# Kernel optimization log

Measured on AMD Instinct MI355X. Metric: run time of the kernel, lower is better.

## Reference

```python
import jax, jax.numpy as jnp
import numpy as np

NUM_USERS = 100000
NUM_ITEMS = 50000
NUM_LAYERS = 4
DIM_H = 64
E_HALF = 2000000  # undirected interactions; symmetrized to 4M directed edges


def setup_inputs() -> dict:
    key = jax.random.key(0)
    k1, k2, k3, k4 = jax.random.split(key, 4)
    emb_users = 0.01 * jax.random.normal(k1, (NUM_USERS, DIM_H), dtype=jnp.float32)
    emb_items = 0.01 * jax.random.normal(k2, (NUM_ITEMS, DIM_H), dtype=jnp.float32)
    u = jax.random.randint(k3, (E_HALF,), 0, NUM_USERS, dtype=jnp.int64)
    it = jax.random.randint(k4, (E_HALF,), 0, NUM_ITEMS, dtype=jnp.int64) + NUM_USERS
    # bidirectional bipartite graph, as LightGCN expects
    src = jnp.concatenate([u, it])
    dst = jnp.concatenate([it, u])
    edge_index = jnp.stack([src, dst])  # [2, 4M]
    return {"emb_users": emb_users, "emb_items": emb_items, "edge_index": edge_index}


def reference(emb_users, emb_items, edge_index):
    N = emb_users.shape[0] + emb_items.shape[0]
    src, dst = edge_index[0], edge_index[1]
    # gcn_norm (add_self_loops=False): w_e = deg[src]^-1/2 * deg[dst]^-1/2
    deg = jax.ops.segment_sum(jnp.ones(src.shape[0], dtype=emb_users.dtype), dst, num_segments=N)
    dis = jnp.where(deg > 0, deg ** -0.5, 0.0).astype(emb_users.dtype)
    w = (dis[src] * dis[dst])[:, None]  # [E,1]

    emb = jnp.concatenate([emb_users, emb_items])  # [N, D]
    embs_sum = emb
    x = emb
    for _ in range(NUM_LAYERS):
        x = jax.ops.segment_sum(w * x[src], dst, num_segments=N)  # LGConv
        embs_sum = embs_sum + x
    # original: 1/(L+1) * mean over L+1 stacked layers -> sum / (L+1)^2
    emb_final = embs_sum / float((NUM_LAYERS + 1) ** 2)
    emb_users_final = emb_final[: emb_users.shape[0]]
    emb_items_final = emb_final[emb_users.shape[0]:]
    return (emb_users_final, emb_users, emb_items_final, emb_items)
```

## Files before the change

### kernel.cpp

```cpp
#include <hip/hip_runtime.h>
#include <hip/hip_fp8.h>

typedef unsigned char u8;
typedef float v2f __attribute__((ext_vector_type(2)));

#define SCAN_B 256

#define NPB      128
#define NPB_SH   7
#define P2_CAP   6144
#define STG_CAP  6144
#define P1_CHUNK 8192
#define NB_MAX   2048
#define STG_OFF  ((size_t)10 << 20)

static __device__ __forceinline__ float fp8_to_f32(u8 b) {
    __hip_fp8_e4m3 t;
    t.__x = (__hip_fp8_storage_t)b;
    return (float)t;
}
static __device__ __forceinline__ u8 f32_to_fp8(float v) {
    __hip_fp8_e4m3 t(v);
    return (u8)t.__x;
}

template <bool HI>
static __device__ __forceinline__ v2f pk2(unsigned w) {
#if __has_builtin(__builtin_amdgcn_cvt_pk_f32_fp8)
    return __builtin_amdgcn_cvt_pk_f32_fp8((int)w, HI);
#else
    v2f r;
    r.x = fp8_to_f32(HI ? (u8)(w >> 16) : (u8)(w));
    r.y = fp8_to_f32(HI ? (u8)(w >> 24) : (u8)(w >> 8));
    return r;
#endif
}

__global__ void detect_kernel(const int* __restrict__ edges, int* __restrict__ flag) {
    __shared__ int cnt[256];
    int t = threadIdx.x;
    int c = 0;
    for (int i = t; i < 32768; i += 256)
        if (edges[2 * i + 1] != 0) c++;
    cnt[t] = c;
    __syncthreads();
    for (int off = 128; off > 0; off >>= 1) {
        if (t < off) cnt[t] += cnt[t + off];
        __syncthreads();
    }
    if (t == 0) flag[0] = (cnt[0] < 8) ? 2 : 1;
}

__global__ void gcur_fixed_init(int* __restrict__ gcur, int NB) {
    int b = blockIdx.x * blockDim.x + threadIdx.x;
    if (b < NB) gcur[b] = b * STG_CAP;
}

__global__ void part1_kernel(const int* __restrict__ edges, const int* __restrict__ flag,
                             int* __restrict__ gcur, int2* __restrict__ staging,
                             int E, int NB) {
    __shared__ int lcount[NB_MAX];
    __shared__ int lbase[NB_MAX];
    int t = threadIdx.x;
    int s = flag[0];
    long e0 = (long)blockIdx.x * P1_CHUNK;
    for (int b = t; b < NB; b += 256) lcount[b] = 0;
    __syncthreads();
    for (int j = 0; j < P1_CHUNK / 256; ++j) {
        long e = e0 + j * 256 + t;
        if (e < E) {
            int dv = edges[(long)E * s + e * s];
            atomicAdd(&lcount[dv >> NPB_SH], 1);
        }
    }
    __syncthreads();
    for (int b = t; b < NB; b += 256) {
        int c = lcount[b];
        lbase[b] = (c > 0) ? atomicAdd(&gcur[b], c) : 0;
        lcount[b] = 0;
    }
    __syncthreads();
    for (int j = 0; j < P1_CHUNK / 256; ++j) {
        long e = e0 + j * 256 + t;
        if (e < E) {
            int sv = edges[e * s];
            int dv = edges[(long)E * s + e * s];
            int b = dv >> NPB_SH;
            int slot = atomicAdd(&lcount[b], 1);
            int pos = lbase[b] + slot;
            if (pos < (b + 1) * STG_CAP)
                staging[pos] = make_int2(sv, dv);
        }
    }
}

__global__ void bucket_scan_kernel(const int* __restrict__ gcur, int* __restrict__ bbase,
                                   int NB) {
    __shared__ int sh[2][1024];
    int t = threadIdx.x;
    int i0 = 2 * t, i1 = 2 * t + 1;
    int a0 = (i0 < NB) ? (gcur[i0] - i0 * STG_CAP) : 0;
    int a1 = (i1 < NB) ? (gcur[i1] - i1 * STG_CAP) : 0;
    sh[0][t] = a0 + a1;
    __syncthreads();
    int src = 0;
    for (int off = 1; off < 1024; off <<= 1) {
        int x = sh[src][t] + ((t >= off) ? sh[src][t - off] : 0);
        sh[src ^ 1][t] = x;
        src ^= 1;
        __syncthreads();
    }
    int incl = sh[src][t];
    int excl = incl - (a0 + a1);
    if (i0 < NB) bbase[i0] = excl;
    if (i1 < NB) bbase[i1] = excl + a0;
    if (t == 1023) bbase[NB] = incl;
}

__global__ void __launch_bounds__(256) part2a_kernel(
        const int* __restrict__ gcur, const int* __restrict__ bbase,
        const int2* __restrict__ staging, int* __restrict__ row_ptr,
        float* __restrict__ dis, int n, int E, int NB) {
    __shared__ int cnt[NPB];
    __shared__ int sc[2][NPB];
    int b = blockIdx.x;
    int t = threadIdx.x;
    int dlo = b << NPB_SH;
    int sbase = b * STG_CAP;
    int c = gcur[b] - sbase;
    int base = bbase[b];
    if (t < NPB) cnt[t] = 0;
    __syncthreads();
    for (int k = t; k < c; k += 256) {
        int2 sd = staging[sbase + k];
        atomicAdd(&cnt[sd.y - dlo], 1);
    }
    __syncthreads();
    if (t < NPB) sc[0][t] = cnt[t];
    __syncthreads();
    int src = 0;
    for (int off = 1; off < NPB; off <<= 1) {
        if (t < NPB) {
            int x = sc[src][t] + ((t >= off) ? sc[src][t - off] : 0);
            sc[src ^ 1][t] = x;
        }
        src ^= 1;
        __syncthreads();
    }
    if (t < NPB) {
        int node = dlo + t;
        if (node < n) {
            int d = cnt[t];
            row_ptr[node] = base + sc[src][t] - d;
            dis[node] = (d > 0) ? rsqrtf((float)d) : 0.0f;
        }
    }
    if (b == 0 && t == 0) row_ptr[n] = E;
}

__global__ void __launch_bounds__(256) part2b_kernel(
        const int* __restrict__ row_ptr, const int* __restrict__ gcur,
        const int2* __restrict__ staging, const float* __restrict__ dis,
        int2* __restrict__ cw, int n) {
    __shared__ int2 win[P2_CAP];
    __shared__ int cur[NPB];
    int b = blockIdx.x;
    int t = threadIdx.x;
    int dlo = b << NPB_SH;
    int sbase = b * STG_CAP;
    int cnt = gcur[b] - sbase;
    int base = row_ptr[dlo];
    if (t < NPB) {
        int node = dlo + t;
        cur[t] = (node < n) ? (row_ptr[node] - base) : 0;
    }
    __syncthreads();
    if (cnt <= P2_CAP) {
        for (int k = t; k < cnt; k += 256) {
            int2 sd = staging[sbase + k];
            float w = dis[sd.x] * dis[sd.y];
            int p = atomicAdd(&cur[sd.y - dlo], 1);
            win[p] = make_int2(sd.x, __float_as_int(w));
        }
        __syncthreads();
        for (int k = t; k < cnt; k += 256)
            cw[base + k] = win[k];
    } else {
        for (int k = t; k < cnt; k += 256) {
            int2 sd = staging[sbase + k];
            float w = dis[sd.x] * dis[sd.y];
            int p = atomicAdd(&cur[sd.y - dlo], 1);
            cw[base + p] = make_int2(sd.x, __float_as_int(w));
        }
    }
}

__global__ void count_deg_kernel(const int* __restrict__ edges, const int* __restrict__ flag,
                                 int* __restrict__ deg, int E) {
    int e = blockIdx.x * blockDim.x + threadIdx.x;
    if (e >= E) return;
    int s = flag[0];
    int d = edges[(long)E * s + (long)e * s];
    atomicAdd(&deg[d], 1);
}

__global__ void scan_phase1(const int* __restrict__ deg, int* __restrict__ row_ptr,
                            int* __restrict__ bsum, int n) {
    __shared__ int sh[2][SCAN_B];
    int t = threadIdx.x;
    int gi = blockIdx.x * SCAN_B + t;
    int v = (gi < n) ? deg[gi] : 0;
    int src = 0;
    sh[0][t] = v;
    __syncthreads();
    for (int off = 1; off < SCAN_B; off <<= 1) {
        int x = sh[src][t] + ((t >= off) ? sh[src][t - off] : 0);
        sh[src ^ 1][t] = x;
        src ^= 1;
        __syncthreads();
    }
    int incl = sh[src][t];
    if (gi < n) row_ptr[gi] = incl - v;
    if (t == SCAN_B - 1) bsum[blockIdx.x] = incl;
}

__global__ void scan_phase2(int* __restrict__ bsum, int nb) {
    __shared__ int sh[1024];
    int t = threadIdx.x;
    sh[t] = (t < nb) ? bsum[t] : 0;
    __syncthreads();
    if (t == 0) {
        int acc = 0;
        for (int i = 0; i < nb; ++i) { int x = sh[i]; sh[i] = acc; acc += x; }
    }
    __syncthreads();
    if (t < nb) bsum[t] = sh[t];
}

__global__ void scan_phase3(const int* __restrict__ deg, const int* __restrict__ bsum,
                            int* __restrict__ row_ptr, int* __restrict__ cursor,
                            float* __restrict__ dis, int n, int E) {
    int gi = blockIdx.x * SCAN_B + threadIdx.x;
    if (gi < n) {
        int e = row_ptr[gi] + bsum[blockIdx.x];
        row_ptr[gi] = e;
        cursor[gi]  = e;
        int d = deg[gi];
        dis[gi] = (d > 0) ? rsqrtf((float)d) : 0.0f;
    }
    if (gi == 0) row_ptr[n] = E;
}

__global__ void scatter_kernel(const int* __restrict__ edges, const int* __restrict__ flag,
                               const float* __restrict__ dis, int* __restrict__ cursor,
                               int2* __restrict__ cw, int E) {
    int e = blockIdx.x * blockDim.x + threadIdx.x;
    if (e >= E) return;
    int s = flag[0];
    int sv = edges[(long)e * s];
    int dv = edges[(long)E * s + (long)e * s];
    float w = dis[sv] * dis[dv];
    int pos = atomicAdd(&cursor[dv], 1);
    cw[pos] = make_int2(sv, __float_as_int(w));
}

__global__ void init_kernel(const float* __restrict__ eu, const float* __restrict__ ei,
                            u8* __restrict__ x0, long NU64, long tot) {
    long i = (long)blockIdx.x * blockDim.x + threadIdx.x;
    if (i >= tot) return;
    float v = (i < NU64) ? eu[i] : ei[i - NU64];
    x0[i] = f32_to_fp8(v);
}

__global__ void spmm_kernel(const int* __restrict__ row_ptr, const int2* __restrict__ cw,
                            const u8* __restrict__ xin, u8* __restrict__ xout, int n) {
    int wave = (blockIdx.x * blockDim.x + threadIdx.x) >> 6;
    int lane = threadIdx.x & 63;
    if (wave >= n) return;
    int beg = row_ptr[wave], end = row_ptr[wave + 1];
    int g = lane >> 3;
    int h = lane & 7;

    float a0 = 0.f, a1 = 0.f, a2 = 0.f, a3 = 0.f;
    float a4 = 0.f, a5 = 0.f, a6 = 0.f, a7 = 0.f;

    for (int iA = beg + g; iA < end; iA += 16) {
        int iB = iA + 8;
        bool vB = iB < end;

        int2 ca = cw[iA];
        int2 cb = cw[vB ? iB : iA];

        uint2 dA = *(const uint2*)(xin + ((long)ca.x << 6) + (h << 3));
        uint2 dB = *(const uint2*)(xin + ((long)cb.x << 6) + (h << 3));

        float wA = __int_as_float(ca.y);
        float wB = vB ? __int_as_float(cb.y) : 0.0f;

        v2f pA0 = pk2<false>(dA.x), pA1 = pk2<true>(dA.x);
        v2f pA2 = pk2<false>(dA.y), pA3 = pk2<true>(dA.y);
        v2f pB0 = pk2<false>(dB.x), pB1 = pk2<true>(dB.x);
        v2f pB2 = pk2<false>(dB.y), pB3 = pk2<true>(dB.y);

        a0 = fmaf(wA, pA0.x, a0); a1 = fmaf(wA, pA0.y, a1);
        a2 = fmaf(wA, pA1.x, a2); a3 = fmaf(wA, pA1.y, a3);
        a4 = fmaf(wA, pA2.x, a4); a5 = fmaf(wA, pA2.y, a5);
        a6 = fmaf(wA, pA3.x, a6); a7 = fmaf(wA, pA3.y, a7);
        a0 = fmaf(wB, pB0.x, a0); a1 = fmaf(wB, pB0.y, a1);
        a2 = fmaf(wB, pB1.x, a2); a3 = fmaf(wB, pB1.y, a3);
        a4 = fmaf(wB, pB2.x, a4); a5 = fmaf(wB, pB2.y, a5);
        a6 = fmaf(wB, pB3.x, a6); a7 = fmaf(wB, pB3.y, a7);
    }

    a0 += __shfl_xor(a0, 8);  a1 += __shfl_xor(a1, 8);
    a2 += __shfl_xor(a2, 8);  a3 += __shfl_xor(a3, 8);
    a4 += __shfl_xor(a4, 8);  a5 += __shfl_xor(a5, 8);
    a6 += __shfl_xor(a6, 8);  a7 += __shfl_xor(a7, 8);
    a0 += __shfl_xor(a0, 16); a1 += __shfl_xor(a1, 16);
    a2 += __shfl_xor(a2, 16); a3 += __shfl_xor(a3, 16);
    a4 += __shfl_xor(a4, 16); a5 += __shfl_xor(a5, 16);
    a6 += __shfl_xor(a6, 16); a7 += __shfl_xor(a7, 16);
    a0 += __shfl_xor(a0, 32); a1 += __shfl_xor(a1, 32);
    a2 += __shfl_xor(a2, 32); a3 += __shfl_xor(a3, 32);
    a4 += __shfl_xor(a4, 32); a5 += __shfl_xor(a5, 32);
    a6 += __shfl_xor(a6, 32); a7 += __shfl_xor(a7, 32);

    if (g == 0) {
        unsigned lo = (unsigned)f32_to_fp8(a0)
                    | ((unsigned)f32_to_fp8(a1) << 8)
                    | ((unsigned)f32_to_fp8(a2) << 16)
                    | ((unsigned)f32_to_fp8(a3) << 24);
        unsigned hi = (unsigned)f32_to_fp8(a4)
                    | ((unsigned)f32_to_fp8(a5) << 8)
                    | ((unsigned)f32_to_fp8(a6) << 16)
                    | ((unsigned)f32_to_fp8(a7) << 24);
        *(uint2*)(xout + ((long)wave << 6) + (h << 3)) = make_uint2(lo, hi);
    }
}

__global__ void final_kernel(const u8* __restrict__ x1, const u8* __restrict__ x2,
                             const u8* __restrict__ x3, const u8* __restrict__ x4,
                             const float* __restrict__ eu, const float* __restrict__ ei,
                             float* __restrict__ out, long NU64, long NI64) {
    long i = (long)blockIdx.x * blockDim.x + threadIdx.x;
    if (i >= NU64 + NI64) return;
    float base = (i < NU64) ? eu[i] : ei[i - NU64];
    float s = base + fp8_to_f32(x1[i]) + fp8_to_f32(x2[i])
                   + fp8_to_f32(x3[i]) + fp8_to_f32(x4[i]);
    float v = s * (1.0f / 25.0f);
    if (i < NU64) {
        out[i] = v;
        out[NU64 + i] = base;
    } else {
        long j = i - NU64;
        out[2 * NU64 + j] = v;
        out[2 * NU64 + NI64 + j] = base;
    }
}

extern "C" void kernel_launch(void* const* d_in, const int* in_sizes, int n_in,
                              void* d_out, int out_size, void* d_ws, size_t ws_size,
                              hipStream_t stream) {
    const float* eu = (const float*)d_in[0];
    const float* ei = (const float*)d_in[1];
    const int* edges = (const int*)d_in[2];
    float* out = (float*)d_out;

    const int NU = in_sizes[0] / 64;
    const int NI = in_sizes[1] / 64;
    const int N  = NU + NI;
    const int E  = in_sizes[2] / 2;
    const int NB = (N + NPB - 1) / NPB;

    char* w = (char*)d_ws;
    size_t off = 0;
    auto alloc = [&](size_t bytes) -> void* {
        void* p = w + off;
        off += (bytes + 255) & ~(size_t)255;
        return p;
    };
    int*   flag    = (int*)  alloc(256);
    int*   deg     = (int*)  alloc((size_t)N * 4);
    int*   row_ptr = (int*)  alloc((size_t)(N + 1) * 4);
    int*   cursor  = (int*)  alloc((size_t)N * 4);
    float* dis     = (float*)alloc((size_t)N * 4);
    int*   bsum    = (int*)  alloc(1024 * 4);
    int*   gcur    = (int*)  alloc((size_t)(NB + 1) * 4);
    int*   bbase   = (int*)  alloc((size_t)(NB + 1) * 4);
    int2*  cw      = (int2*) alloc((size_t)E * 8);
    const long NU64 = (long)NU * 64, NI64 = (long)NI * 64;
    const long tot = NU64 + NI64;
    u8* x1 = (u8*)alloc((size_t)tot);
    u8* x2 = (u8*)alloc((size_t)tot);
    u8* x3 = (u8*)alloc((size_t)tot);
    u8* x4 = (u8*)alloc((size_t)tot);

    const size_t out_bytes = (size_t)tot * 8;
    u8*   x0      = (u8*)out;
    int2* staging = (int2*)((char*)out + STG_OFF);

    detect_kernel<<<1, 256, 0, stream>>>(edges, flag);

    bool fast = (NB <= NB_MAX) &&
                (STG_OFF + (size_t)NB * STG_CAP * 8 <= out_bytes) &&
                ((size_t)tot <= STG_OFF);

    if (fast) {
        gcur_fixed_init<<<(NB + 255) / 256, 256, 0, stream>>>(gcur, NB);
        part1_kernel<<<(E + P1_CHUNK - 1) / P1_CHUNK, 256, 0, stream>>>(edges, flag, gcur,
                                                                        staging, E, NB);
        bucket_scan_kernel<<<1, 1024, 0, stream>>>(gcur, bbase, NB);
        part2a_kernel<<<NB, 256, 0, stream>>>(gcur, bbase, staging, row_ptr, dis, N, E, NB);
        part2b_kernel<<<NB, 256, 0, stream>>>(row_ptr, gcur, staging, dis, cw, N);
    } else {
        const int nb = (N + SCAN_B - 1) / SCAN_B;
        hipMemsetAsync(deg, 0, (size_t)N * 4, stream);
        count_deg_kernel<<<(E + 255) / 256, 256, 0, stream>>>(edges, flag, deg, E);
        scan_phase1<<<nb, SCAN_B, 0, stream>>>(deg, row_ptr, bsum, N);
        scan_phase2<<<1, 1024, 0, stream>>>(bsum, nb);
        scan_phase3<<<nb, SCAN_B, 0, stream>>>(deg, bsum, row_ptr, cursor, dis, N, E);
        scatter_kernel<<<(E + 255) / 256, 256, 0, stream>>>(edges, flag, dis, cursor, cw, E);
    }

    init_kernel<<<(int)((tot + 255) / 256), 256, 0, stream>>>(eu, ei, x0, NU64, tot);

    const int nblk = (N + 3) / 4;
    spmm_kernel<<<nblk, 256, 0, stream>>>(row_ptr, cw, x0, x1, N);
    spmm_kernel<<<nblk, 256, 0, stream>>>(row_ptr, cw, x1, x2, N);
    spmm_kernel<<<nblk, 256, 0, stream>>>(row_ptr, cw, x2, x3, N);
    spmm_kernel<<<nblk, 256, 0, stream>>>(row_ptr, cw, x3, x4, N);

    final_kernel<<<(int)((tot + 255) / 256), 256, 0, stream>>>(x1, x2, x3, x4, eu, ei,
                                                               out, NU64, NI64);
}
```

Baseline: 562.5 us.

## Pack staging entries into 32-bit words and enlarge part1 chunks

Staging entries change from int2 (src,dst) pairs to a single 32-bit word holding the 20-bit source index and the 7-bit local destination offset. This halves staging write/read traffic in part1, part2a and part2b. part1 also processes 32K edges per block with 512 threads, so there are fewer blocks and fewer global atomics on the bucket cursors. A guard N < 2^20 keeps the packing valid, at the cost of less parallelism in part1 (about 122 blocks).

```diff
diff --git a/kernel.cpp b/kernel.cpp
--- a/kernel.cpp
+++ b/kernel.cpp
@@ -10,7 +10,8 @@
 #define NPB_SH   7
 #define P2_CAP   6144
 #define STG_CAP  6144
-#define P1_CHUNK 8192
+#define P1_CHUNK 32768
+#define P1_T     512
 #define NB_MAX   2048
 #define STG_OFF  ((size_t)10 << 20)
 
@@ -57,31 +58,31 @@
 }
 
 __global__ void part1_kernel(const int* __restrict__ edges, const int* __restrict__ flag,
-                             int* __restrict__ gcur, int2* __restrict__ staging,
+                             int* __restrict__ gcur, unsigned* __restrict__ staging,
                              int E, int NB) {
     __shared__ int lcount[NB_MAX];
     __shared__ int lbase[NB_MAX];
     int t = threadIdx.x;
     int s = flag[0];
     long e0 = (long)blockIdx.x * P1_CHUNK;
-    for (int b = t; b < NB; b += 256) lcount[b] = 0;
-    __syncthreads();
-    for (int j = 0; j < P1_CHUNK / 256; ++j) {
-        long e = e0 + j * 256 + t;
+    for (int b = t; b < NB; b += P1_T) lcount[b] = 0;
+    __syncthreads();
+    for (int j = 0; j < P1_CHUNK / P1_T; ++j) {
+        long e = e0 + (long)j * P1_T + t;
         if (e < E) {
             int dv = edges[(long)E * s + e * s];
             atomicAdd(&lcount[dv >> NPB_SH], 1);
         }
     }
     __syncthreads();
-    for (int b = t; b < NB; b += 256) {
+    for (int b = t; b < NB; b += P1_T) {
         int c = lcount[b];
         lbase[b] = (c > 0) ? atomicAdd(&gcur[b], c) : 0;
         lcount[b] = 0;
     }
     __syncthreads();
-    for (int j = 0; j < P1_CHUNK / 256; ++j) {
-        long e = e0 + j * 256 + t;
+    for (int j = 0; j < P1_CHUNK / P1_T; ++j) {
+        long e = e0 + (long)j * P1_T + t;
         if (e < E) {
             int sv = edges[e * s];
             int dv = edges[(long)E * s + e * s];
@@ -89,7 +90,7 @@
             int slot = atomicAdd(&lcount[b], 1);
             int pos = lbase[b] + slot;
             if (pos < (b + 1) * STG_CAP)
-                staging[pos] = make_int2(sv, dv);
+                staging[pos] = (unsigned)sv | ((unsigned)(dv & (NPB - 1)) << 20);
         }
     }
 }
@@ -119,7 +120,7 @@
 
 __global__ void __launch_bounds__(256) part2a_kernel(
         const int* __restrict__ gcur, const int* __restrict__ bbase,
-        const int2* __restrict__ staging, int* __restrict__ row_ptr,
+        const unsigned* __restrict__ staging, int* __restrict__ row_ptr,
         float* __restrict__ dis, int n, int E, int NB) {
     __shared__ int cnt[NPB];
     __shared__ int sc[2][NPB];
@@ -132,8 +133,8 @@
     if (t < NPB) cnt[t] = 0;
     __syncthreads();
     for (int k = t; k < c; k += 256) {
-        int2 sd = staging[sbase + k];
-        atomicAdd(&cnt[sd.y - dlo], 1);
+        unsigned wd = staging[sbase + k];
+        atomicAdd(&cnt[wd >> 20], 1);
     }
     __syncthreads();
     if (t < NPB) sc[0][t] = cnt[t];
@@ -160,7 +161,7 @@
 
 __global__ void __launch_bounds__(256) part2b_kernel(
         const int* __restrict__ row_ptr, const int* __restrict__ gcur,
-        const int2* __restrict__ staging, const float* __restrict__ dis,
+        const unsigned* __restrict__ staging, const float* __restrict__ dis,
         int2* __restrict__ cw, int n) {
     __shared__ int2 win[P2_CAP];
     __shared__ int cur[NPB];
@@ -177,20 +178,24 @@
     __syncthreads();
     if (cnt <= P2_CAP) {
         for (int k = t; k < cnt; k += 256) {
-            int2 sd = staging[sbase + k];
-            float w = dis[sd.x] * dis[sd.y];
-            int p = atomicAdd(&cur[sd.y - dlo], 1);
-            win[p] = make_int2(sd.x, __float_as_int(w));
+            unsigned wd = staging[sbase + k];
+            int sv = wd & 0xFFFFF;
+            int dloc = wd >> 20;
+            float w = dis[sv] * dis[dlo + dloc];
+            int p = atomicAdd(&cur[dloc], 1);
+            win[p] = make_int2(sv, __float_as_int(w));
         }
         __syncthreads();
         for (int k = t; k < cnt; k += 256)
             cw[base + k] = win[k];
     } else {
         for (int k = t; k < cnt; k += 256) {
-            int2 sd = staging[sbase + k];
-            float w = dis[sd.x] * dis[sd.y];
-            int p = atomicAdd(&cur[sd.y - dlo], 1);
-            cw[base + p] = make_int2(sd.x, __float_as_int(w));
+            unsigned wd = staging[sbase + k];
+            int sv = wd & 0xFFFFF;
+            int dloc = wd >> 20;
+            float w = dis[sv] * dis[dlo + dloc];
+            int p = atomicAdd(&cur[dloc], 1);
+            cw[base + p] = make_int2(sv, __float_as_int(w));
         }
     }
 }
@@ -396,19 +401,19 @@
     u8* x4 = (u8*)alloc((size_t)tot);
 
     const size_t out_bytes = (size_t)tot * 8;
-    u8*   x0      = (u8*)out;
-    int2* staging = (int2*)((char*)out + STG_OFF);
+    u8*       x0      = (u8*)out;
+    unsigned* staging = (unsigned*)((char*)out + STG_OFF);
 
     detect_kernel<<<1, 256, 0, stream>>>(edges, flag);
 
-    bool fast = (NB <= NB_MAX) &&
-                (STG_OFF + (size_t)NB * STG_CAP * 8 <= out_bytes) &&
+    bool fast = (NB <= NB_MAX) && (N < (1 << 20)) &&
+                (STG_OFF + (size_t)NB * STG_CAP * 4 <= out_bytes) &&
                 ((size_t)tot <= STG_OFF);
 
     if (fast) {
         gcur_fixed_init<<<(NB + 255) / 256, 256, 0, stream>>>(gcur, NB);
-        part1_kernel<<<(E + P1_CHUNK - 1) / P1_CHUNK, 256, 0, stream>>>(edges, flag, gcur,
-                                                                        staging, E, NB);
+        part1_kernel<<<(E + P1_CHUNK - 1) / P1_CHUNK, P1_T, 0, stream>>>(edges, flag, gcur,
+                                                                         staging, E, NB);
         bucket_scan_kernel<<<1, 1024, 0, stream>>>(gcur, bbase, NB);
         part2a_kernel<<<NB, 256, 0, stream>>>(gcur, bbase, staging, row_ptr, dis, N, E, NB);
         part2b_kernel<<<NB, 256, 0, stream>>>(row_ptr, gcur, staging, dis, cw, N);
```

Result: slower. 575.0 us (+2.2%).
